# Performance work log

Measured on AMD Instinct MI355X. Metric: run time of the kernel, lower is better.

The kernel has to match this reference:

```python
import jax, jax.numpy as jnp
import numpy as np

GRAN = 4      # mask_spatial_granularity
STRIDE = 1    # dilate_stride
PAD = 1       # ExpandMask padding -> 3x3 all-ones dilation kernel


def setup_inputs() -> dict:
    key = jax.random.key(0)
    k1, k2, k3 = jax.random.split(key, 3)
    B, C, H, W = 32, 64, 112, 112
    G = 4
    mh, mw = H // STRIDE // GRAN, W // STRIDE // GRAN
    x = jax.random.normal(k1, (B, C, H, W), jnp.float32)
    weight = jax.random.normal(k2, (2 * G, C), jnp.float32) * 0.05  # 1x1 conv
    bias = jnp.zeros((2 * G,), jnp.float32).at[:G].set(5.0).at[G + 1:].set(1.0)
    # standard gumbel(0,1) noise for gumbel_softmax
    u = jax.random.uniform(k3, (B, 2, G, mh, mw), jnp.float32, 1e-10, 1.0)
    gumbel = -jnp.log(-jnp.log(u))
    temperature = jnp.float32(1.0)
    return {"x": x, "weight": weight, "bias": bias, "gumbel": gumbel,
            "temperature": temperature}


def reference(x, weight, bias, gumbel, temperature):
    B, C, H, W = x.shape
    G = weight.shape[0] // 2
    mh, mw = H // STRIDE // GRAN, W // STRIDE // GRAN   # mask grid (28,28)
    fh, fw = H // STRIDE, W // STRIDE                   # feature size (112,112)

    # adaptive_avg_pool2d (H,W evenly divisible by mask grid)
    m = x.reshape(B, C, mh, H // mh, mw, W // mw).mean(axis=(3, 5))
    flops = C * mh * mw
    # 1x1 conv
    m = jnp.einsum('bchw,oc->bohw', m, weight) + bias[None, :, None, None]
    flops += (weight.shape[0] * weight.shape[1] + weight.shape[1]) * mh * mw

    # gumbel_softmax over dim=1 with hard=True (straight-through)
    logits = m.reshape(B, 2, G, mh, mw)
    y_soft = jax.nn.softmax((logits + gumbel) / temperature, axis=1)
    idx = jnp.argmax(y_soft, axis=1)
    y_hard = jax.nn.one_hot(idx, 2, axis=1, dtype=y_soft.dtype)
    y = y_hard - jax.lax.stop_gradient(y_soft) + y_soft
    mask = y[:, 0]                                      # [B,G,mh,mw]
    sparsity = mask.sum() / mask.size

    # F.interpolate(size=feature_size), default mode='nearest' with integer factor
    mask = jnp.repeat(jnp.repeat(mask, fh // mh, axis=2), fw // mw, axis=3)

    # ExpandMask (stride=1): 3x3 all-ones full (cross-channel) conv, then >0.5
    dk = jnp.ones((G, G, 1 + 2 * PAD, 1 + 2 * PAD), mask.dtype)
    dil = jax.lax.conv_general_dilated(
        mask, dk, window_strides=(1, 1), padding=((PAD, PAD), (PAD, PAD)),
        dimension_numbers=('NCHW', 'OIHW', 'NCHW'))
    mask_dil = dil > 0.5
    sparsity_dil = jnp.mean(mask_dil.astype(jnp.float32))

    return mask, mask_dil, sparsity, sparsity_dil, flops
```

## Files before the change

kernel.cpp:

```cpp
#include <hip/hip_runtime.h>

#define MH 28
#define MW 28
#define CC 64
#define GG 4
#define NB 32

typedef float vf4 __attribute__((ext_vector_type(4)));

__device__ __forceinline__ int xcd_swizzle(int phys) {
    return (phys & 7) * 112 + (phys >> 3);
}


__global__ __launch_bounds__(256, 3) void masker_d1(
    const float* __restrict__ x, const float* __restrict__ w,
    const float* __restrict__ bias, const float* __restrict__ gum,
    unsigned char* __restrict__ coarse, unsigned char* __restrict__ anyb)
{
    const int blk = xcd_swizzle(blockIdx.x);
    int b = blk / MH, ch = blk - (blk / MH) * MH, t = threadIdx.x;
    __shared__ float pooled[CC][MW];
    __shared__ float wlds[8 * CC];
    __shared__ float logits[8][MW];
    __shared__ unsigned char mlds[GG][MW];

    float g0 = 0.f, g1 = 0.f, bo = 0.f;
    if (t < GG * MW) {
        int g = t / MW, cw = t - g * MW;
        g0 = gum[((((size_t)b * 2 + 0) * GG + g) * MH + ch) * MW + cw];
        g1 = gum[((((size_t)b * 2 + 1) * GG + g) * MH + ch) * MW + cw];
    }
    if (t < 8 * MW) bo = bias[t / MW];
    if (t < 128) ((float4*)wlds)[t] = ((const float4*)w)[t];

    const float* xb = x + (size_t)b * CC * 12544 + (size_t)(4 * ch) * 112;

    vf4 r[7][4];
    #pragma unroll
    for (int k = 0; k < 7; ++k) {
        int p  = t + 256 * k;
        int c  = p / MW;
        int cw = p - c * MW;
        const vf4* base = (const vf4*)(xb + (size_t)c * 12544 + 4 * cw);
        #pragma unroll
        for (int hh = 0; hh < 4; ++hh)
            r[k][hh] = __builtin_nontemporal_load(base + hh * 28);
    }
    #pragma unroll
    for (int k = 0; k < 7; ++k) {
        int p  = t + 256 * k;
        int c  = p / MW;
        int cw = p - c * MW;
        float s = 0.f;
        #pragma unroll
        for (int hh = 0; hh < 4; ++hh)
            s += r[k][hh].x + r[k][hh].y + r[k][hh].z + r[k][hh].w;
        pooled[c][cw] = s * 0.0625f;
    }
    __syncthreads();

    if (t < 8 * MW) {
        int o = t / MW, cw = t - o * MW;
        float acc = bo;
        #pragma unroll
        for (int c = 0; c < CC; ++c)
            acc += pooled[c][cw] * wlds[o * CC + c];
        logits[o][cw] = acc;
    }
    __syncthreads();

    if (t < GG * MW) {
        int g = t / MW, cw = t - g * MW;
        unsigned char mv = (logits[g][cw] + g0 >= logits[g + 4][cw] + g1) ? 1u : 0u;
        mlds[g][cw] = mv;
        coarse[(((size_t)b * GG + g) * MH + ch) * MW + cw] = mv;
    }
    __syncthreads();
    if (t < MW)
        anyb[((size_t)b * MH + ch) * MW + t] =
            mlds[0][t] | mlds[1][t] | mlds[2][t] | mlds[3][t];
}

__global__ __launch_bounds__(256) void masker_d2(
    const unsigned char* __restrict__ coarse,
    const unsigned char* __restrict__ anyb,
    float* __restrict__ out_mask, float* __restrict__ out_dil,
    uint2* __restrict__ slots)
{
    const int blk = xcd_swizzle(blockIdx.x);
    int b = blk / MH, ch = blk - (blk / MH) * MH, t = threadIdx.x;
    __shared__ float carr[GG][MW];
    __shared__ float R[3][MW + 2];
    __shared__ unsigned int sm[4], sd[4];

    unsigned int local_m = 0;
    if (t < GG * MW) {
        int g = t / MW, cw = t - g * MW;
        unsigned char mv = coarse[(((size_t)b * GG + g) * MH + ch) * MW + cw];
        carr[g][cw] = (float)mv;
        local_m = mv;
    }
    if (t < MW) {
        float a  = (float)anyb[((size_t)b * MH + ch) * MW + t];
        float am = (ch > 0)      ? (float)anyb[((size_t)b * MH + ch - 1) * MW + t] : 0.f;
        float ap = (ch < MH - 1) ? (float)anyb[((size_t)b * MH + ch + 1) * MW + t] : 0.f;
        R[0][t + 1] = fmaxf(a, am);
        R[1][t + 1] = a;
        R[2][t + 1] = fmaxf(a, ap);
    }
    if (t < 3) { R[t][0] = 0.f; R[t][MW + 1] = 0.f; }
    __syncthreads();

    unsigned int local_d = 0;
    #pragma unroll
    for (int k = 0; k < 7; ++k) {
        int idx = t + 256 * k;
        int g   = idx / 448;
        int rem = idx - g * 448;
        int hh  = rem / 112;
        int wfi = rem - hh * 112;
        int cw  = wfi >> 2;
        int wm  = wfi & 3;
        int rv  = (hh == 0) ? 0 : (hh == 3 ? 2 : 1);
        float d;
        if (wm == 0)      d = fmaxf(R[rv][cw],     R[rv][cw + 1]);
        else if (wm == 3) d = fmaxf(R[rv][cw + 1], R[rv][cw + 2]);
        else              d = R[rv][cw + 1];
        float mv = carr[g][cw];
        size_t o = (((size_t)b * GG + g) * 112 + (4 * ch + hh)) * 112 + wfi;
        __builtin_nontemporal_store(mv, &out_mask[o]);
        __builtin_nontemporal_store(d,  &out_dil[o]);
        local_d += (d > 0.5f) ? 1u : 0u;
    }

    #pragma unroll
    for (int off = 32; off; off >>= 1) {
        local_m += __shfl_down(local_m, off);
        local_d += __shfl_down(local_d, off);
    }
    if ((t & 63) == 0) { sm[t >> 6] = local_m; sd[t >> 6] = local_d; }
    __syncthreads();
    if (t == 0) {
        uint2 v;
        v.x = sm[0] + sm[1] + sm[2] + sm[3];
        v.y = sd[0] + sd[1] + sd[2] + sd[3];
        slots[blk] = v;
    }
}

__global__ __launch_bounds__(256) void masker_d3(
    const uint2* __restrict__ slots, float* __restrict__ out_scalars)
{
    int t = threadIdx.x;
    unsigned int m = 0, d = 0;
    for (int i = t; i < NB * MH; i += 256) { uint2 v = slots[i]; m += v.x; d += v.y; }
    #pragma unroll
    for (int off = 32; off; off >>= 1) {
        m += __shfl_down(m, off);
        d += __shfl_down(d, off);
    }
    __shared__ unsigned int sm[4], sd[4];
    if ((t & 63) == 0) { sm[t >> 6] = m; sd[t >> 6] = d; }
    __syncthreads();
    if (t == 0) {
        out_scalars[0] = (float)(sm[0] + sm[1] + sm[2] + sm[3]) / 100352.0f;
        out_scalars[1] = (float)(sd[0] + sd[1] + sd[2] + sd[3]) / 1605632.0f;
        out_scalars[2] = 501760.0f;
    }
}

extern "C" void kernel_launch(void* const* d_in, const int* in_sizes, int n_in,
                              void* d_out, int out_size, void* d_ws, size_t ws_size,
                              hipStream_t stream) {
    const float* x    = (const float*)d_in[0];
    const float* w    = (const float*)d_in[1];
    const float* bias = (const float*)d_in[2];
    const float* gum  = (const float*)d_in[3];

    float* out = (float*)d_out;
    const size_t n_mask = (size_t)NB * GG * 112 * 112;

    uint2*         slots  = (uint2*)d_ws;
    unsigned char* coarse = (unsigned char*)d_ws + 8192;
    unsigned char* anyb   = (unsigned char*)d_ws + 8192 + 100352;

    dim3 grid(NB * MH);
    masker_d1<<<grid, 256, 0, stream>>>(x, w, bias, gum, coarse, anyb);
    masker_d2<<<grid, 256, 0, stream>>>(coarse, anyb, out, out + n_mask, slots);
    masker_d3<<<1, 256, 0, stream>>>(slots, out + 2 * n_mask);
}
```

Measured before the change: 28.13 us.

## Write upsampled mask directly from pooling kernel, drop coarse mask buffer

The first kernel now computes the hard mask and writes the full-resolution upsampled mask output itself, along with the per-block mask count. This removes the intermediate coarse-mask buffer round trip and splits the output stores across two kernels. The second kernel now only writes the dilated mask. The cost is extra store work in the memory-bound pooling kernel, which may lengthen it.

```diff
diff --git a/kernel.cpp b/kernel.cpp
--- a/kernel.cpp
+++ b/kernel.cpp
@@ -16,14 +16,17 @@
 __global__ __launch_bounds__(256, 3) void masker_d1(
     const float* __restrict__ x, const float* __restrict__ w,
     const float* __restrict__ bias, const float* __restrict__ gum,
-    unsigned char* __restrict__ coarse, unsigned char* __restrict__ anyb)
+    float* __restrict__ out_mask, unsigned char* __restrict__ anyb,
+    unsigned int* __restrict__ slotm)
 {
     const int blk = xcd_swizzle(blockIdx.x);
-    int b = blk / MH, ch = blk - (blk / MH) * MH, t = threadIdx.x;
+    const int b = blk / MH, ch = blk - (blk / MH) * MH;
+    const int t = threadIdx.x;
     __shared__ float pooled[CC][MW];
     __shared__ float wlds[8 * CC];
     __shared__ float logits[8][MW];
-    __shared__ unsigned char mlds[GG][MW];
+    __shared__ float decf[GG][MW];
+    __shared__ unsigned int sm[4];
 
     float g0 = 0.f, g1 = 0.f, bo = 0.f;
     if (t < GG * MW) {
@@ -35,7 +38,6 @@
     if (t < 128) ((float4*)wlds)[t] = ((const float4*)w)[t];
 
     const float* xb = x + (size_t)b * CC * 12544 + (size_t)(4 * ch) * 112;
-
     vf4 r[7][4];
     #pragma unroll
     for (int k = 0; k < 7; ++k) {
@@ -70,41 +72,54 @@
     }
     __syncthreads();
 
-    if (t < GG * MW) {
-        int g = t / MW, cw = t - g * MW;
-        unsigned char mv = (logits[g][cw] + g0 >= logits[g + 4][cw] + g1) ? 1u : 0u;
-        mlds[g][cw] = mv;
-        coarse[(((size_t)b * GG + g) * MH + ch) * MW + cw] = mv;
-    }
-    __syncthreads();
-    if (t < MW)
-        anyb[((size_t)b * MH + ch) * MW + t] =
-            mlds[0][t] | mlds[1][t] | mlds[2][t] | mlds[3][t];
-}
-
-__global__ __launch_bounds__(256) void masker_d2(
-    const unsigned char* __restrict__ coarse,
-    const unsigned char* __restrict__ anyb,
-    float* __restrict__ out_mask, float* __restrict__ out_dil,
-    uint2* __restrict__ slots)
-{
-    const int blk = xcd_swizzle(blockIdx.x);
-    int b = blk / MH, ch = blk - (blk / MH) * MH, t = threadIdx.x;
-    __shared__ float carr[GG][MW];
-    __shared__ float R[3][MW + 2];
-    __shared__ unsigned int sm[4], sd[4];
-
     unsigned int local_m = 0;
     if (t < GG * MW) {
         int g = t / MW, cw = t - g * MW;
-        unsigned char mv = coarse[(((size_t)b * GG + g) * MH + ch) * MW + cw];
-        carr[g][cw] = (float)mv;
-        local_m = mv;
-    }
+        float mv = (logits[g][cw] + g0 >= logits[g + 4][cw] + g1) ? 1.f : 0.f;
+        decf[g][cw] = mv;
+        local_m = (unsigned int)mv;
+    }
+    __syncthreads();
+
     if (t < MW) {
-        float a  = (float)anyb[((size_t)b * MH + ch) * MW + t];
-        float am = (ch > 0)      ? (float)anyb[((size_t)b * MH + ch - 1) * MW + t] : 0.f;
-        float ap = (ch < MH - 1) ? (float)anyb[((size_t)b * MH + ch + 1) * MW + t] : 0.f;
+        float a = fmaxf(fmaxf(decf[0][t], decf[1][t]), fmaxf(decf[2][t], decf[3][t]));
+        anyb[(size_t)blk * MW + t] = (unsigned char)a;
+    }
+
+    #pragma unroll
+    for (int k = 0; k < 7; ++k) {
+        int idx = t + 256 * k;
+        int g   = idx / 448;
+        int rem = idx - g * 448;
+        int hh  = rem / 112;
+        int wfi = rem - hh * 112;
+        float mv = decf[g][wfi >> 2];
+        size_t o = (((size_t)b * GG + g) * 112 + (4 * ch + hh)) * 112 + wfi;
+        __builtin_nontemporal_store(mv, &out_mask[o]);
+    }
+
+    #pragma unroll
+    for (int off = 32; off; off >>= 1)
+        local_m += __shfl_down(local_m, off);
+    if ((t & 63) == 0) sm[t >> 6] = local_m;
+    __syncthreads();
+    if (t == 0) slotm[blk] = sm[0] + sm[1] + sm[2] + sm[3];
+}
+
+__global__ __launch_bounds__(256) void masker_d2(
+    const unsigned char* __restrict__ anyb,
+    float* __restrict__ out_dil, unsigned int* __restrict__ slotd)
+{
+    const int blk = xcd_swizzle(blockIdx.x);
+    const int b = blk / MH, ch = blk - (blk / MH) * MH;
+    const int t = threadIdx.x;
+    __shared__ float R[3][MW + 2];
+    __shared__ unsigned int sd[4];
+
+    if (t < MW) {
+        float a  = (float)anyb[(size_t)blk * MW + t];
+        float am = (ch > 0)      ? (float)anyb[(size_t)(blk - 1) * MW + t] : 0.f;
+        float ap = (ch < MH - 1) ? (float)anyb[(size_t)(blk + 1) * MW + t] : 0.f;
         R[0][t + 1] = fmaxf(a, am);
         R[1][t + 1] = a;
         R[2][t + 1] = fmaxf(a, ap);
@@ -127,34 +142,27 @@
         if (wm == 0)      d = fmaxf(R[rv][cw],     R[rv][cw + 1]);
         else if (wm == 3) d = fmaxf(R[rv][cw + 1], R[rv][cw + 2]);
         else              d = R[rv][cw + 1];
-        float mv = carr[g][cw];
         size_t o = (((size_t)b * GG + g) * 112 + (4 * ch + hh)) * 112 + wfi;
-        __builtin_nontemporal_store(mv, &out_mask[o]);
-        __builtin_nontemporal_store(d,  &out_dil[o]);
+        __builtin_nontemporal_store(d, &out_dil[o]);
         local_d += (d > 0.5f) ? 1u : 0u;
     }
 
     #pragma unroll
-    for (int off = 32; off; off >>= 1) {
-        local_m += __shfl_down(local_m, off);
+    for (int off = 32; off; off >>= 1)
         local_d += __shfl_down(local_d, off);
-    }
-    if ((t & 63) == 0) { sm[t >> 6] = local_m; sd[t >> 6] = local_d; }
-    __syncthreads();
-    if (t == 0) {
-        uint2 v;
-        v.x = sm[0] + sm[1] + sm[2] + sm[3];
-        v.y = sd[0] + sd[1] + sd[2] + sd[3];
-        slots[blk] = v;
-    }
+    if ((t & 63) == 0) sd[t >> 6] = local_d;
+    __syncthreads();
+    if (t == 0) slotd[blk] = sd[0] + sd[1] + sd[2] + sd[3];
 }
 
 __global__ __launch_bounds__(256) void masker_d3(
-    const uint2* __restrict__ slots, float* __restrict__ out_scalars)
+    const unsigned int* __restrict__ slotm,
+    const unsigned int* __restrict__ slotd,
+    float* __restrict__ out_scalars)
 {
     int t = threadIdx.x;
     unsigned int m = 0, d = 0;
-    for (int i = t; i < NB * MH; i += 256) { uint2 v = slots[i]; m += v.x; d += v.y; }
+    for (int i = t; i < NB * MH; i += 256) { m += slotm[i]; d += slotd[i]; }
     #pragma unroll
     for (int off = 32; off; off >>= 1) {
         m += __shfl_down(m, off);
@@ -181,12 +189,12 @@
     float* out = (float*)d_out;
     const size_t n_mask = (size_t)NB * GG * 112 * 112;
 
-    uint2*         slots  = (uint2*)d_ws;
-    unsigned char* coarse = (unsigned char*)d_ws + 8192;
-    unsigned char* anyb   = (unsigned char*)d_ws + 8192 + 100352;
+    unsigned int*  slotm = (unsigned int*)d_ws;
+    unsigned int*  slotd = (unsigned int*)((char*)d_ws + 4096);
+    unsigned char* anyb  = (unsigned char*)d_ws + 8192;
 
     dim3 grid(NB * MH);
-    masker_d1<<<grid, 256, 0, stream>>>(x, w, bias, gum, coarse, anyb);
-    masker_d2<<<grid, 256, 0, stream>>>(coarse, anyb, out, out + n_mask, slots);
-    masker_d3<<<1, 256, 0, stream>>>(slots, out + 2 * n_mask);
-}
+    masker_d1<<<grid, 256, 0, stream>>>(x, w, bias, gum, out, anyb, slotm);
+    masker_d2<<<grid, 256, 0, stream>>>(anyb, out + n_mask, slotd);
+    masker_d3<<<1, 256, 0, stream>>>(slotm, slotd, out + 2 * n_mask);
+}
```

New measurement: 30.25 us. +7.5%, slower.
